# Optimization experiments

Hardware: AMD Instinct MI355X
Metric: run time of the kernel (lower is better)

Reference implementation:

```python
import jax, jax.numpy as jnp
import numpy as np

T, WQ, WS, C, H, W = 2, 75, 25, 640, 10, 10
WAY, SHOT = 5, 5
HID = C // 16
SCALE_VALUE = 30.0
ATTEN_SCALE_VALUE = 50.0
FROM_VALUE = 0.5
VALUE_INTERVAL = 0.3
BN_EPS = 1e-5
NORM_EPS = 1e-12


def _leaky(x):
    return jnp.where(x >= 0, x, 0.2 * x)


def _l2norm(x, axis):
    n = jnp.sqrt(jnp.sum(x * x, axis=axis, keepdims=True))
    return x / jnp.maximum(n, NORM_EPS)


def _embed(x, W_conv, bn_gamma, bn_beta, bn_mean, bn_var):
    # 1x1 conv (no bias) + eval-mode BatchNorm + LeakyReLU(0.2)
    # x: [t, n, c, h, w] -> [t, n, c, h, w]
    y = jnp.einsum('oc,tnchw->tnohw', W_conv, x)
    inv = bn_gamma / jnp.sqrt(bn_var + BN_EPS)
    y = y * inv[:, None, None] + (bn_beta - bn_mean * inv)[:, None, None]
    return _leaky(y)


def setup_inputs() -> dict:
    key = jax.random.key(0)
    ks = jax.random.split(key, 5)
    return {
        'query_feat': jax.random.normal(ks[0], (T, WQ, C, H, W), dtype=jnp.float32),
        'support_feat': jax.random.normal(ks[1], (T, WS, C, H, W), dtype=jnp.float32),
        'W_conv': jax.random.normal(ks[2], (C, C), dtype=jnp.float32) * 0.02,
        'bn_gamma': jnp.ones((C,), jnp.float32),
        'bn_beta': jnp.zeros((C,), jnp.float32),
        'bn_mean': jnp.zeros((C,), jnp.float32),
        'bn_var': jnp.ones((C,), jnp.float32),
        'psi_w1': jax.random.normal(ks[3], (C, HID), dtype=jnp.float32) * 0.04,
        'psi_b1': jnp.zeros((HID,), jnp.float32),
        'psi_w2': jax.random.normal(ks[4], (HID, 1), dtype=jnp.float32) * 0.15,
        'psi_b2': jnp.zeros((1,), jnp.float32),
        'way_num': WAY,
        'shot_num': SHOT,
    }


def reference(query_feat, support_feat, W_conv, bn_gamma, bn_beta, bn_mean, bn_var,
              psi_w1, psi_b1, psi_w2, psi_b2, way_num, shot_num):
    t, wq, c, h, w = query_feat.shape
    ws = support_feat.shape[1]
    hw = h * w

    # embedded + normalized features for the gated branch
    w_query = _embed(query_feat, W_conv, bn_gamma, bn_beta, bn_mean, bn_var)
    w_query = w_query.reshape(t, wq, c, hw).transpose(0, 1, 3, 2)      # [t, wq, hw, c]
    w_support = _embed(support_feat, W_conv, bn_gamma, bn_beta, bn_mean, bn_var)
    w_support = w_support.reshape(t, ws, c, hw).transpose(0, 2, 1, 3).reshape(t, c, ws * hw)
    w_query = _l2norm(w_query, axis=3)
    w_support = _l2norm(w_support, axis=1)

    # cosine similarity of embedded features: [t, wq, hw, ws*hw]
    f_x = jnp.einsum('tqpc,tck->tqpk', w_query, w_support)

    # AEAModule: per-location adaptive threshold from f_psi MLP
    hid = _leaky(w_query @ psi_w1 + psi_b1)                            # [t, wq, hw, HID]
    clamp_value = jax.nn.sigmoid(hid @ psi_w2 + psi_b2) * VALUE_INTERVAL + FROM_VALUE
    clamp_fx = jax.nn.sigmoid(ATTEN_SCALE_VALUE * (f_x - clamp_value))
    atten_score = clamp_fx / jnp.maximum(
        jnp.sum(jnp.abs(clamp_fx), axis=-1, keepdims=True), NORM_EPS)  # L1 normalize

    # raw-feature cosine similarity
    qf = _l2norm(query_feat.reshape(t, wq, c, hw).transpose(0, 1, 3, 2), axis=3)
    sf = _l2norm(support_feat.reshape(t, ws, c, hw).transpose(0, 2, 1, 3).reshape(t, c, ws * hw), axis=1)
    match_score = jnp.einsum('tqpc,tck->tqpk', qf, sf)                 # [t, wq, hw, ws*hw]

    # gate, regroup support axis into (way, shot, hw_s), reduce
    ams = (atten_score * match_score).reshape(t, wq, hw, way_num, shot_num, hw)
    score = ams.sum(axis=-1).mean(axis=(2, 4)) * SCALE_VALUE           # [t, wq, way]
    return score
```

## Files before the change

kernel.cpp:

```cpp
#include <hip/hip_runtime.h>
#include <stdint.h>

#define T_    2
#define WQ_   75
#define WS_   25
#define C_    640
#define HW_   100
#define HID_  40
#define WAY_  5
#define QP_   (WQ_*HW_)
#define SP_   (WS_*HW_)
#define NPT_  59
#define QT_   (NPT_*128)
#define KPAD_ 512
#define KROWS_ (WAY_*KPAD_)
#define C8_   (C_/8)
#define BM_   256

typedef _Float16 f16;
typedef _Float16 f16x8 __attribute__((ext_vector_type(8)));
typedef _Float16 f16x4 __attribute__((ext_vector_type(4)));
typedef _Float16 f16x16 __attribute__((ext_vector_type(16)));
typedef float    f32x4 __attribute__((ext_vector_type(4)));
typedef float    f32x16 __attribute__((ext_vector_type(16)));
typedef uint32_t u32;

__device__ __forceinline__ void gl_lds16(const f16* g, f16* l) {
  __builtin_amdgcn_global_load_lds(
      (const __attribute__((address_space(1))) u32*)g,
      (__attribute__((address_space(3))) u32*)l, 16, 0, 0);
}

__global__ __launch_bounds__(512) void k0_invnorm(
    const float* __restrict__ q, const float* __restrict__ s,
    float* __restrict__ rq_inv, float* __restrict__ rq_nrm,
    float* __restrict__ rs_inv, float* __restrict__ rs_nrm) {
  __shared__ float part[4][128];
  int b = blockIdx.x;
  int t = b / (WQ_ + WS_);
  int n = b % (WQ_ + WS_);
  int tid = threadIdx.x;
  int seg = tid >> 7, p = tid & 127;
  const float* base; float* oi; float* on; size_t idx;
  if (n < WQ_) {
    base = q + ((size_t)(t*WQ_ + n))*C_*HW_;
    idx = (size_t)t*QT_ + n*HW_ + p; oi = rq_inv; on = rq_nrm;
  } else {
    int m = n - WQ_;
    base = s + ((size_t)(t*WS_ + m))*C_*HW_;
    idx = (size_t)t*SP_ + m*HW_ + p; oi = rs_inv; on = rs_nrm;
  }
  float ss = 0.f;
  if (p < HW_) {
    for (int c = seg*160; c < seg*160 + 160; ++c) {
      float v = base[c*HW_ + p]; ss += v*v;
    }
  }
  part[seg][p] = ss;
  __syncthreads();
  if (seg == 0 && p < HW_) {
    float tot = part[0][p] + part[1][p] + part[2][p] + part[3][p];
    float nrm = fmaxf(sqrtf(tot), 1e-12f);
    oi[idx] = 1.f/nrm; on[idx] = nrm;
  }
}

__global__ __launch_bounds__(256) void kw_packW(
    const float* __restrict__ W, const float* __restrict__ w1,
    f16* __restrict__ Wr, f16* __restrict__ Wt8, f16* __restrict__ w1t) {
  int idx = blockIdx.x*256 + threadIdx.x;
  if (idx < C_*C8_) {
    int o = idx / C8_, c8 = idx % C8_;
    f16x8 v;
#pragma unroll
    for (int i = 0; i < 8; ++i) v[i] = (f16)W[(size_t)o*C_ + c8*8 + i];
    *reinterpret_cast<f16x8*>(Wr + (size_t)o*C_ + c8*8) = v;
    *reinterpret_cast<f16x8*>(Wt8 + ((size_t)c8*C_ + o)*8) = v;
  } else if (idx < C_*C8_ + 48*C8_) {
    int k2 = idx - C_*C8_;
    int h = k2 / C8_, c8 = k2 % C8_;
    f16x8 v;
#pragma unroll
    for (int i = 0; i < 8; ++i)
      v[i] = (h < HID_) ? (f16)w1[(size_t)(c8*8+i)*HID_ + h] : (f16)0.f;
    *reinterpret_cast<f16x8*>(w1t + (size_t)h*C_ + c8*8) = v;
  }
}

__global__ __launch_bounds__(256) void k1_pack_qraw(
    const float* __restrict__ q, const float* __restrict__ rq_inv,
    f16* __restrict__ Bq_raw) {
  int b = blockIdx.x;
  int ct = b % 10; b /= 10;
  int qq = b % WQ_; int t = b / WQ_;
  int c0 = ct*64;
  __shared__ float lds[64*HW_];
  const float4* s4 = reinterpret_cast<const float4*>(
      q + (((size_t)(t*WQ_ + qq))*C_ + c0)*HW_);
  float4* l4 = reinterpret_cast<float4*>(lds);
  for (int i = threadIdx.x; i < 64*HW_/4; i += 256) l4[i] = s4[i];
  __syncthreads();
  for (int ch = threadIdx.x; ch < 8*HW_; ch += 256) {
    int lc8 = ch / HW_, p = ch % HW_;
    float inv = rq_inv[(size_t)t*QT_ + qq*HW_ + p];
    f16x8 v;
#pragma unroll
    for (int i = 0; i < 8; ++i) v[i] = (f16)(lds[(lc8*8 + i)*HW_ + p] * inv);
    *reinterpret_cast<f16x8*>(
        Bq_raw + ((size_t)(t*C8_ + c0/8 + lc8)*QT_ + qq*HW_ + p)*8) = v;
  }
}

__global__ __launch_bounds__(256) void k2_pack_sraw(
    const float* __restrict__ s, const float* __restrict__ rs_inv,
    f16* __restrict__ As_raw) {
  int b = blockIdx.x;
  int ct = b % 10; b /= 10;
  int n = b % WS_; int t = b / WS_;
  int c0 = ct*64;
  __shared__ float lds[64*HW_];
  const float4* s4 = reinterpret_cast<const float4*>(
      s + (((size_t)(t*WS_ + n))*C_ + c0)*HW_);
  float4* l4 = reinterpret_cast<float4*>(lds);
  for (int i = threadIdx.x; i < 64*HW_/4; i += 256) l4[i] = s4[i];
  __syncthreads();
  for (int ch = threadIdx.x; ch < HW_*8; ch += 256) {
    int p = ch / 8, cc = ch % 8;
    float inv = rs_inv[t*SP_ + n*HW_ + p];
    f16x8 v;
#pragma unroll
    for (int i = 0; i < 8; ++i) v[i] = (f16)(lds[(cc*8 + i)*HW_ + p] * inv);
    int k = n*HW_ + p;
    int way = k / 500, ki = k % 500;
    size_t row = (size_t)way*KPAD_ + ki;
    *reinterpret_cast<f16x8*>(As_raw + ((size_t)(t*C8_ + c0/8 + cc)*KROWS_ + row)*8) = v;
  }
}

__global__ __launch_bounds__(512) void k3_embed_support(
    const f16* __restrict__ As_raw, const f16* __restrict__ Wt8,
    const float* __restrict__ rs_nrm,
    const float* __restrict__ g, const float* __restrict__ be,
    const float* __restrict__ mu, const float* __restrict__ va,
    f16* __restrict__ As_emb) {
  int b = blockIdx.x;
  int t = b / (KROWS_/32);
  int row0 = (b % (KROWS_/32)) * 32;
  int tid = threadIdx.x, wv = tid >> 6, lane = tid & 63;
  int mf = wv & 1, nh = wv >> 1;
  __shared__ f16 Alds[32*32];
  __shared__ f16 Blds[32*C_];
  __shared__ float rowss[32];
  f32x4 acc[10];
#pragma unroll
  for (int i = 0; i < 10; ++i) acc[i] = (f32x4){0.f,0.f,0.f,0.f};

  for (int cs = 0; cs < 20; ++cs) {
    if (tid < 128) {
      int c8l = tid >> 5, r = tid & 31;
      *reinterpret_cast<f16x8*>(Alds + (c8l*32 + r)*8) =
        *reinterpret_cast<const f16x8*>(
            As_raw + ((size_t)(t*C8_ + cs*4 + c8l)*KROWS_ + row0 + r)*8);
    }
    const f16x8* bsrc = reinterpret_cast<const f16x8*>(Wt8 + (size_t)(cs*4)*C_*8);
    f16x8* bdst = reinterpret_cast<f16x8*>(Blds);
    for (int i = tid; i < 4*C_; i += 512) bdst[i] = bsrc[i];
    __syncthreads();
    f16x8 a = *reinterpret_cast<const f16x8*>(
        Alds + ((lane>>4)*32 + mf*16 + (lane&15))*8);
#pragma unroll
    for (int nf = 0; nf < 10; ++nf) {
      int o = nh*160 + nf*16 + (lane & 15);
      f16x8 bf = *reinterpret_cast<const f16x8*>(Blds + (((lane>>4)*C_) + o)*8);
      acc[nf] = __builtin_amdgcn_mfma_f32_16x16x32_f16(a, bf, acc[nf], 0, 0, 0);
    }
    __syncthreads();
  }

  if (tid < 32) rowss[tid] = 0.f;
  __syncthreads();
  int rg = lane >> 4, cl = lane & 15;
  int lrow = mf*16 + rg*4;
  int prow = row0 + lrow;
#pragma unroll
  for (int j = 0; j < 4; ++j) {
    int pr = prow + j;
    int way = pr / KPAD_, ki = pr - way*KPAD_;
    bool valid = ki < 500;
    float nrm = valid ? rs_nrm[t*SP_ + way*500 + ki] : 0.f;
    float ssum = 0.f;
#pragma unroll
    for (int nf = 0; nf < 10; ++nf) {
      int o = nh*160 + nf*16 + cl;
      float inv = g[o] / sqrtf(va[o] + 1e-5f);
      float sh = be[o] - mu[o]*inv;
      float y = acc[nf][j]*nrm*inv + sh;
      y = (y >= 0.f) ? y : 0.2f*y;
      if (!valid) y = 0.f;
      acc[nf][j] = y;
      ssum += y*y;
    }
#pragma unroll
    for (int m = 1; m < 16; m <<= 1) ssum += __shfl_xor(ssum, m);
    if (cl == 0) atomicAdd(&rowss[lrow + j], ssum);
  }
  __syncthreads();
#pragma unroll
  for (int j = 0; j < 4; ++j) {
    int pr = prow + j;
    int ki = pr - (pr / KPAD_)*KPAD_;
    if (ki >= 500) continue;
    float invn = 1.f / fmaxf(sqrtf(rowss[lrow + j]), 1e-12f);
#pragma unroll
    for (int nf = 0; nf < 10; ++nf) {
      int o = nh*160 + nf*16 + cl;
      As_emb[((size_t)(t*C8_ + (o>>3))*KROWS_ + pr)*8 + (o&7)] = (f16)(acc[nf][j]*invn);
    }
  }
}

__global__ __launch_bounds__(256, 3) void k4_embed_query(
    const f16* __restrict__ Wr, const f16* __restrict__ Bq_raw,
    const float* __restrict__ rq_nrm,
    const float* __restrict__ g, const float* __restrict__ be,
    const float* __restrict__ mu, const float* __restrict__ va,
    f16* __restrict__ Bq_emb) {
  __shared__ f16 Ab[3][128*32];
  __shared__ f16 Bb[3][4*128*8];
  int b = blockIdx.x;
  int ot = b % 5; int m = b / 5;
  int pt = m % NPT_; int t = m / NPT_;
  int o0 = ot*128;
  int tid = threadIdx.x, w = tid >> 6, lane = tid & 63;
  int la_r = lane >> 2, la_c = lane & 3;

  auto stage = [&](int buf, int cs) {
#pragma unroll
    for (int i = 0; i < 2; ++i) {
      int ca = w*2 + i;
      int r = ca*16 + la_r;
      int sc = la_c ^ (r & 3);
      gl_lds16(Wr + (size_t)(o0 + r)*C_ + cs*32 + sc*8, &Ab[buf][ca*512]);
    }
#pragma unroll
    for (int i = 0; i < 2; ++i) {
      int cb = w*2 + i;
      int c8l = cb >> 1;
      size_t src = ((size_t)(t*C8_ + cs*4 + c8l)*QT_ + pt*128 + (cb&1)*64 + lane)*8;
      gl_lds16(Bq_raw + src, &Bb[buf][(c8l*128 + (cb&1)*64)*8]);
    }
  };

  f32x4 acc[2][8];
#pragma unroll
  for (int a = 0; a < 2; ++a)
#pragma unroll
    for (int n = 0; n < 8; ++n) acc[a][n] = (f32x4){0.f,0.f,0.f,0.f};

  stage(0, 0);
  stage(1, 1);
  for (int cs = 0; cs < 20; ++cs) {
    int buf = cs % 3;
    if (cs < 19) asm volatile("s_waitcnt vmcnt(4)" ::: "memory");
    else         asm volatile("s_waitcnt vmcnt(0)" ::: "memory");
    __builtin_amdgcn_s_barrier();
    if (cs < 18) stage((cs+2)%3, cs+2);
    __builtin_amdgcn_s_setprio(1);
    f16x8 fa[2];
#pragma unroll
    for (int mi = 0; mi < 2; ++mi) {
      int R = w*32 + mi*16 + (lane & 15);
      int sc = (lane >> 4) ^ (R & 3);
      fa[mi] = *reinterpret_cast<const f16x8*>(&Ab[buf][R*32 + sc*8]);
    }
#pragma unroll
    for (int nf = 0; nf < 8; ++nf) {
      f16x8 fb = *reinterpret_cast<const f16x8*>(
          &Bb[buf][((lane>>4)*128 + nf*16 + (lane&15))*8]);
#pragma unroll
      for (int mi = 0; mi < 2; ++mi)
        acc[mi][nf] = __builtin_amdgcn_mfma_f32_16x16x32_f16(fa[mi], fb, acc[mi][nf], 0, 0, 0);
    }
    __builtin_amdgcn_s_setprio(0);
  }

#pragma unroll
  for (int mi = 0; mi < 2; ++mi) {
    int obase = o0 + w*32 + mi*16 + (lane>>4)*4;
    float inv4[4], sh4[4];
#pragma unroll
    for (int j = 0; j < 4; ++j) {
      int o = obase + j;
      inv4[j] = g[o] / sqrtf(va[o] + 1e-5f);
      sh4[j] = be[o] - mu[o]*inv4[j];
    }
#pragma unroll
    for (int nf = 0; nf < 8; ++nf) {
      size_t gp = (size_t)pt*128 + nf*16 + (lane & 15);
      float nrmv = rq_nrm[(size_t)t*QT_ + gp];
      f16x4 vv;
#pragma unroll
      for (int j = 0; j < 4; ++j) {
        float y = (nrmv > 0.f) ? (acc[mi][nf][j]*nrmv*inv4[j] + sh4[j]) : 0.f;
        y = (y >= 0.f) ? y : 0.2f*y;
        vv[j] = (f16)y;
      }
      *reinterpret_cast<f16x4*>(
          &Bq_emb[((size_t)(t*C8_ + (obase>>3))*QT_ + gp)*8 + (obase&7)]) = vv;
    }
  }
}

__global__ __launch_bounds__(256) void k5_colnorm_psi(
    const f16* __restrict__ Bq_emb, const f16* __restrict__ w1t,
    const float* __restrict__ b1, const float* __restrict__ w2,
    const float* __restrict__ b2, float* __restrict__ cv,
    float* __restrict__ invq) {
  __shared__ float ssA[2][128];
  __shared__ float invs[128];
  __shared__ float hidL[48*128];
  int bq = blockIdx.x;
  int pt = bq % NPT_, t = bq / NPT_;
  int tid = threadIdx.x, w = tid >> 6, lane = tid & 63;
  size_t pbase = (size_t)pt*128;

  auto bptr = [&](int c8, int pp) -> const f16* {
    return Bq_emb + ((size_t)(t*C8_ + c8)*QT_ + pbase + pp)*8;
  };

  {
    int h2 = tid >> 7, pp = tid & 127;
    float ss = 0.f;
    for (int c8 = h2*40; c8 < h2*40 + 40; ++c8) {
      f16x8 v = *reinterpret_cast<const f16x8*>(bptr(c8, pp));
#pragma unroll
      for (int i = 0; i < 8; ++i) { float x = (float)v[i]; ss += x*x; }
    }
    ssA[h2][pp] = ss;
  }
  for (int i = tid; i < 48*128; i += 256) hidL[i] = 0.f;
  __syncthreads();
  if (tid < 128) {
    float ss = ssA[0][tid] + ssA[1][tid];
    float inv = (ss > 0.f) ? (1.f / fmaxf(sqrtf(ss), 1e-12f)) : 0.f;
    invs[tid] = inv;
    invq[(size_t)t*QT_ + pbase + tid] = inv;
  }

  f32x4 acc[3][8];
#pragma unroll
  for (int a = 0; a < 3; ++a)
#pragma unroll
    for (int n = 0; n < 8; ++n) acc[a][n] = (f32x4){0.f,0.f,0.f,0.f};
  for (int r = 0; r < 5; ++r) {
    int cs = w + r*4;
    f16x8 fa[3];
#pragma unroll
    for (int mf = 0; mf < 3; ++mf) {
      int R = mf*16 + (lane & 15);
      fa[mf] = *reinterpret_cast<const f16x8*>(&w1t[(size_t)R*C_ + cs*32 + (lane>>4)*8]);
    }
#pragma unroll
    for (int nf = 0; nf < 8; ++nf) {
      f16x8 fb = *reinterpret_cast<const f16x8*>(
          bptr(cs*4 + (lane>>4), nf*16 + (lane&15)));
#pragma unroll
      for (int mf = 0; mf < 3; ++mf)
        acc[mf][nf] = __builtin_amdgcn_mfma_f32_16x16x32_f16(fa[mf], fb, acc[mf][nf], 0, 0, 0);
    }
  }
  __syncthreads();
  for (int rr = 0; rr < 4; ++rr) {
    if (w == rr) {
#pragma unroll
      for (int mf = 0; mf < 3; ++mf)
#pragma unroll
        for (int nf = 0; nf < 8; ++nf)
#pragma unroll
          for (int j = 0; j < 4; ++j) {
            int row = mf*16 + (lane>>4)*4 + j;
            int col = nf*16 + (lane & 15);
            hidL[row*128 + col] += acc[mf][nf][j];
          }
    }
    __syncthreads();
  }
  if (tid < 128) {
    float inv = invs[tid];
    float z = b2[0];
    for (int h = 0; h < HID_; ++h) {
      float hv = hidL[h*128 + tid]*inv + b1[h];
      hv = (hv >= 0.f) ? hv : 0.2f*hv;
      z += hv*w2[h];
    }
    cv[(size_t)t*QT_ + pbase + tid] = 0.3f/(1.f + __expf(-z)) + 0.5f;
  }
}

__global__ __launch_bounds__(256, 2) void k6_main(
    const f16* __restrict__ As_emb, const f16* __restrict__ As_raw,
    const f16* __restrict__ Bq_emb, const f16* __restrict__ Bq_raw,
    const float* __restrict__ cv, const float* __restrict__ invq,
    float* __restrict__ Spart, float* __restrict__ L1part) {
  __shared__ f16 Ab[3][4*BM_*8];
  __shared__ f16 Bb[3][4*128*8];
  __shared__ float cvs[128], iqs[128], Ss[128], L1s[128];

  int bid = blockIdx.x;
  int xcd = bid & 7, j0 = bid >> 3;
  int l = (xcd < 4) ? xcd*148 + j0 : 592 + (xcd-4)*147 + j0;
  int wk = l % 10; int m = l / 10;
  int pt = m % NPT_; int t = m / NPT_;
  int way = wk >> 1, kt = wk & 1;

  int tid = threadIdx.x, w = tid >> 6, lane = tid & 63;
  if (tid < 128) {
    cvs[tid] = cv[(size_t)t*QT_ + pt*128 + tid];
    iqs[tid] = invq[(size_t)t*QT_ + pt*128 + tid];
    Ss[tid] = 0.f; L1s[tid] = 0.f;
  }
  int wrow0 = w*64;
  size_t rowb = (size_t)way*KPAD_ + (size_t)kt*BM_;

  const size_t aoff = ((size_t)(t*C8_ + w)*KROWS_ + rowb + lane)*8;
  const size_t boff = ((size_t)(t*C8_ + w)*QT_ + pt*128 + lane)*8;
  const f16* pA = As_raw + aoff;
  const f16* pB = Bq_raw + boff;
  const f16* pA1 = As_emb + aoff;
  const f16* pB1 = Bq_emb + boff;
  const int CS_A = 4*KROWS_*8;
  const int CS_B = 4*QT_*8;

  auto stage = [&](int buf, const f16* a, const f16* bsrc) {
    f16* da = &Ab[buf][(size_t)w*BM_*8];
    f16* db = &Bb[buf][(size_t)w*128*8];
    gl_lds16(a,        da);
    gl_lds16(a + 512,  da + 512);
    gl_lds16(a + 1024, da + 1024);
    gl_lds16(a + 1536, da + 1536);
    gl_lds16(bsrc,       db);
    gl_lds16(bsrc + 512, db + 512);
  };

  f32x16 acc[2][4];
  f16x16 mtc[2][4];
#pragma unroll
  for (int mi = 0; mi < 2; ++mi)
#pragma unroll
    for (int nf = 0; nf < 4; ++nf) acc[mi][nf] = (f32x16)(0.f);
  float Sl[4] = {0,0,0,0}, L1l[4] = {0,0,0,0};

  stage(0, pA, pB); pA += CS_A; pB += CS_B;
  stage(1, pA, pB); pA += CS_A; pB += CS_B;

  for (int ph = 0; ph < 40; ++ph) {
    if (ph == 18) { pA = pA1; pB = pB1; }
    int buf = ph % 3;
    if (ph < 39) asm volatile("s_waitcnt vmcnt(6)" ::: "memory");
    else         asm volatile("s_waitcnt vmcnt(0)" ::: "memory");
    __builtin_amdgcn_s_barrier();
    if (ph < 38) { stage((ph+2)%3, pA, pB); pA += CS_A; pB += CS_B; }
    __builtin_amdgcn_s_setprio(1);
    const f16* Abuf = Ab[buf];
    const f16* Bbuf = Bb[buf];
    int r0 = wrow0 + (lane & 31);
#pragma unroll
    for (int ks = 0; ks < 2; ++ks) {
      int c8l = ks*2 + (lane >> 5);
      f16x8 fa0 = *reinterpret_cast<const f16x8*>(&Abuf[(c8l*BM_ + r0)*8]);
      f16x8 fa1 = *reinterpret_cast<const f16x8*>(&Abuf[(c8l*BM_ + r0 + 32)*8]);
#pragma unroll
      for (int nf = 0; nf < 4; ++nf) {
        f16x8 fb = *reinterpret_cast<const f16x8*>(
            &Bbuf[(c8l*128 + nf*32 + (lane & 31))*8]);
        acc[0][nf] = __builtin_amdgcn_mfma_f32_32x32x16_f16(fa0, fb, acc[0][nf], 0, 0, 0);
        acc[1][nf] = __builtin_amdgcn_mfma_f32_32x32x16_f16(fa1, fb, acc[1][nf], 0, 0, 0);
      }
    }
    __builtin_amdgcn_s_setprio(0);

    if (ph == 19) {
#pragma unroll
      for (int mi = 0; mi < 2; ++mi)
#pragma unroll
        for (int nf = 0; nf < 4; ++nf)
#pragma unroll
          for (int jj = 0; jj < 16; ++jj) {
            mtc[mi][nf][jj] = (f16)fminf(fmaxf(acc[mi][nf][jj], -8.f), 8.f);
            acc[mi][nf][jj] = 0.f;
          }
    } else if (ph == 39) {
#pragma unroll
      for (int nf = 0; nf < 4; ++nf) {
        int col = nf*32 + (lane & 31);
        float cvv = cvs[col];
        float iq = iqs[col];
#pragma unroll
        for (int mi = 0; mi < 2; ++mi)
#pragma unroll
          for (int jj = 0; jj < 16; ++jj) {
            float fx = acc[mi][nf][jj] * iq;
            float sg = 1.f/(1.f + __expf(-50.f*(fx - cvv)));
            Sl[nf]  += sg * (float)mtc[mi][nf][jj];
            L1l[nf] += sg;
          }
      }
    }
  }

#pragma unroll
  for (int nf = 0; nf < 4; ++nf) {
    float vs = Sl[nf] + __shfl_xor(Sl[nf], 32);
    float vl = L1l[nf] + __shfl_xor(L1l[nf], 32);
    if (lane < 32) {
      atomicAdd(&Ss[nf*32 + lane], vs);
      atomicAdd(&L1s[nf*32 + lane], vl);
    }
  }
  __syncthreads();
  if (tid < 128) {
    size_t o = ((size_t)((t*WAY_ + way)*2 + kt))*QT_ + (size_t)pt*128 + tid;
    Spart[o] = Ss[tid]; L1part[o] = L1s[tid];
  }
}

__global__ __launch_bounds__(128) void k7_reduce(
    const float* __restrict__ Spart, const float* __restrict__ L1part,
    float* __restrict__ out) {
  int b = blockIdx.x;
  int t = b / WQ_, q = b % WQ_;
  int tid = threadIdx.x;
  __shared__ float red[128];
  float contrib[WAY_] = {0,0,0,0,0};
  if (tid < HW_) {
    size_t p = (size_t)t*0 + (size_t)q*HW_ + tid;
    float l1 = 0.f;
#pragma unroll
    for (int w = 0; w < WAY_; ++w)
#pragma unroll
      for (int k = 0; k < 2; ++k)
        l1 += L1part[((size_t)((t*WAY_ + w)*2 + k))*QT_ + p];
    l1 = fmaxf(l1, 1e-12f);
#pragma unroll
    for (int w = 0; w < WAY_; ++w) {
      float sv = 0.f;
#pragma unroll
      for (int k = 0; k < 2; ++k)
        sv += Spart[((size_t)((t*WAY_ + w)*2 + k))*QT_ + p];
      contrib[w] = sv / l1;
    }
  }
#pragma unroll
  for (int w = 0; w < WAY_; ++w) {
    red[tid] = contrib[w];
    __syncthreads();
    for (int off = 64; off > 0; off >>= 1) {
      if (tid < off) red[tid] += red[tid + off];
      __syncthreads();
    }
    if (tid == 0) out[b*WAY_ + w] = red[0] * 30.f / (float)(HW_*5);
    __syncthreads();
  }
}

extern "C" void kernel_launch(void* const* d_in, const int* in_sizes, int n_in,
                              void* d_out, int out_size, void* d_ws, size_t ws_size,
                              hipStream_t stream) {
  (void)in_sizes; (void)n_in; (void)out_size; (void)ws_size;
  const float* q  = (const float*)d_in[0];
  const float* s  = (const float*)d_in[1];
  const float* W  = (const float*)d_in[2];
  const float* g  = (const float*)d_in[3];
  const float* be = (const float*)d_in[4];
  const float* mu = (const float*)d_in[5];
  const float* va = (const float*)d_in[6];
  const float* w1 = (const float*)d_in[7];
  const float* b1 = (const float*)d_in[8];
  const float* w2 = (const float*)d_in[9];
  const float* b2 = (const float*)d_in[10];
  float* out = (float*)d_out;
  char* ws = (char*)d_ws;

  size_t off = 0;
  auto nxt = [&](size_t bytes) { size_t o = off; off += (bytes + 255) & ~(size_t)255; return o; };
  float* rq_inv = (float*)(ws + nxt((size_t)T_*QT_*4));
  float* rq_nrm = (float*)(ws + nxt((size_t)T_*QT_*4));
  float* rs_inv = (float*)(ws + nxt((size_t)T_*SP_*4));
  float* rs_nrm = (float*)(ws + nxt((size_t)T_*SP_*4));
  f16* Wr     = (f16*)(ws + nxt((size_t)C_*C_*2));
  f16* Wt8    = (f16*)(ws + nxt((size_t)C_*C_*2));
  f16* w1t    = (f16*)(ws + nxt((size_t)48*C_*2));
  f16* As_raw = (f16*)(ws + nxt((size_t)T_*KROWS_*C_*2));
  f16* As_emb = (f16*)(ws + nxt((size_t)T_*KROWS_*C_*2));
  f16* Bq_raw = (f16*)(ws + nxt((size_t)T_*C8_*QT_*8*2));
  f16* Bq_emb = (f16*)(ws + nxt((size_t)T_*C8_*QT_*8*2));
  float* cvp    = (float*)(ws + nxt((size_t)T_*QT_*4));
  float* invq   = (float*)(ws + nxt((size_t)T_*QT_*4));
  float* Spart  = (float*)(ws + nxt((size_t)T_*WAY_*2*QT_*4));
  float* L1part = (float*)(ws + nxt((size_t)T_*WAY_*2*QT_*4));

  hipMemsetAsync(As_raw, 0, (size_t)T_*KROWS_*C_*2, stream);
  hipMemsetAsync(As_emb, 0, (size_t)T_*KROWS_*C_*2, stream);
  hipMemsetAsync(Bq_raw, 0, (size_t)T_*C8_*QT_*8*2, stream);
  hipMemsetAsync(rq_inv, 0, (size_t)T_*QT_*4, stream);
  hipMemsetAsync(rq_nrm, 0, (size_t)T_*QT_*4, stream);

  k0_invnorm<<<T_*(WQ_+WS_), 512, 0, stream>>>(q, s, rq_inv, rq_nrm, rs_inv, rs_nrm);
  kw_packW<<<(C_*C8_ + 48*C8_ + 255)/256, 256, 0, stream>>>(W, w1, Wr, Wt8, w1t);
  k1_pack_qraw<<<T_*WQ_*10, 256, 0, stream>>>(q, rq_inv, Bq_raw);
  k2_pack_sraw<<<T_*WS_*10, 256, 0, stream>>>(s, rs_inv, As_raw);
  k3_embed_support<<<T_*(KROWS_/32), 512, 0, stream>>>(As_raw, Wt8, rs_nrm, g, be, mu, va, As_emb);
  k4_embed_query<<<T_*5*NPT_, 256, 0, stream>>>(Wr, Bq_raw, rq_nrm, g, be, mu, va, Bq_emb);
  k5_colnorm_psi<<<T_*NPT_, 256, 0, stream>>>(Bq_emb, w1t, b1, w2, b2, cvp, invq);
  k6_main<<<1180, 256, 0, stream>>>(As_emb, As_raw, Bq_emb, Bq_raw, cvp, invq, Spart, L1part);
  k7_reduce<<<T_*WQ_, 128, 0, stream>>>(Spart, L1part, out);
}
```

Measured before the change: 304.0 us.

## Widen main GEMM tile to 256x256 with 512-thread blocks and replace memsets

The main similarity kernel now computes a 256x256 output tile per block using 8 waves, which halves the number of blocks and doubles reuse of each staged A/B tile from LDS. The query padding is raised from 59 to 60 tiles of 128 so 256-wide tiles divide evenly, and the XCD block remapping is simplified. The full-buffer hipMemsetAsync calls are replaced by a small kernel that zeroes only the padding regions, and the support embed kernel now writes its padded rows instead of skipping them. Risks are lower occupancy (one block per CU) and some extra padded work.

```diff
diff --git a/kernel.cpp b/kernel.cpp
--- a/kernel.cpp
+++ b/kernel.cpp
@@ -10,12 +10,13 @@
 #define WAY_  5
 #define QP_   (WQ_*HW_)
 #define SP_   (WS_*HW_)
-#define NPT_  59
+#define NPT_  60
 #define QT_   (NPT_*128)
 #define KPAD_ 512
 #define KROWS_ (WAY_*KPAD_)
 #define C8_   (C_/8)
 #define BM_   256
+#define BN_   256
 
 typedef _Float16 f16;
 typedef _Float16 f16x8 __attribute__((ext_vector_type(8)));
@@ -29,6 +30,34 @@
   __builtin_amdgcn_global_load_lds(
       (const __attribute__((address_space(1))) u32*)g,
       (__attribute__((address_space(3))) u32*)l, 16, 0, 0);
+}
+
+__global__ __launch_bounds__(256) void kpad(
+    f16* __restrict__ Bq_raw, f16* __restrict__ As_raw,
+    float* __restrict__ rq_inv, float* __restrict__ rq_nrm) {
+  int idx = blockIdx.x*256 + threadIdx.x;
+  const float4 z4 = make_float4(0.f, 0.f, 0.f, 0.f);
+  if (idx < T_*C8_*(QT_-QP_)) {
+    int pp = idx % (QT_-QP_); int m = idx / (QT_-QP_);
+    int c8 = m % C8_; int t = m / C8_;
+    *reinterpret_cast<float4*>(Bq_raw + ((size_t)(t*C8_+c8)*QT_ + QP_ + pp)*8) = z4;
+    return;
+  }
+  int i2 = idx - T_*C8_*(QT_-QP_);
+  if (i2 < T_*C8_*WAY_*12) {
+    int r = i2 % 12; int m = i2 / 12;
+    int wy = m % WAY_; m /= WAY_;
+    int c8 = m % C8_; int t = m / C8_;
+    *reinterpret_cast<float4*>(
+        As_raw + ((size_t)(t*C8_+c8)*KROWS_ + (size_t)wy*KPAD_ + 500 + r)*8) = z4;
+    return;
+  }
+  int i3 = i2 - T_*C8_*WAY_*12;
+  if (i3 < T_*(QT_-QP_)) {
+    int pp = i3 % (QT_-QP_); int t = i3 / (QT_-QP_);
+    rq_inv[(size_t)t*QT_ + QP_ + pp] = 0.f;
+    rq_nrm[(size_t)t*QT_ + QP_ + pp] = 0.f;
+  }
 }
 
 __global__ __launch_bounds__(512) void k0_invnorm(
@@ -208,8 +237,6 @@
 #pragma unroll
   for (int j = 0; j < 4; ++j) {
     int pr = prow + j;
-    int ki = pr - (pr / KPAD_)*KPAD_;
-    if (ki >= 500) continue;
     float invn = 1.f / fmaxf(sqrtf(rowss[lrow + j]), 1e-12f);
 #pragma unroll
     for (int nf = 0; nf < 10; ++nf) {
@@ -397,33 +424,33 @@
   }
 }
 
-__global__ __launch_bounds__(256, 2) void k6_main(
+__global__ __launch_bounds__(512, 1) void k6_main(
     const f16* __restrict__ As_emb, const f16* __restrict__ As_raw,
     const f16* __restrict__ Bq_emb, const f16* __restrict__ Bq_raw,
     const float* __restrict__ cv, const float* __restrict__ invq,
     float* __restrict__ Spart, float* __restrict__ L1part) {
   __shared__ f16 Ab[3][4*BM_*8];
-  __shared__ f16 Bb[3][4*128*8];
-  __shared__ float cvs[128], iqs[128], Ss[128], L1s[128];
+  __shared__ f16 Bb[3][4*BN_*8];
+  __shared__ float cvs[BN_], iqs[BN_], Ss[BN_], L1s[BN_];
 
   int bid = blockIdx.x;
-  int xcd = bid & 7, j0 = bid >> 3;
-  int l = (xcd < 4) ? xcd*148 + j0 : 592 + (xcd-4)*147 + j0;
+  int l = (bid & 7)*75 + (bid >> 3);
   int wk = l % 10; int m = l / 10;
-  int pt = m % NPT_; int t = m / NPT_;
+  int pt = m % 30; int t = m / 30;
   int way = wk >> 1, kt = wk & 1;
 
   int tid = threadIdx.x, w = tid >> 6, lane = tid & 63;
-  if (tid < 128) {
-    cvs[tid] = cv[(size_t)t*QT_ + pt*128 + tid];
-    iqs[tid] = invq[(size_t)t*QT_ + pt*128 + tid];
+  if (tid < BN_) {
+    cvs[tid] = cv[(size_t)t*QT_ + pt*256 + tid];
+    iqs[tid] = invq[(size_t)t*QT_ + pt*256 + tid];
     Ss[tid] = 0.f; L1s[tid] = 0.f;
   }
-  int wrow0 = w*64;
+  int wr0 = (w & 3)*64;
+  int wc0 = (w >> 2)*128;
   size_t rowb = (size_t)way*KPAD_ + (size_t)kt*BM_;
 
-  const size_t aoff = ((size_t)(t*C8_ + w)*KROWS_ + rowb + lane)*8;
-  const size_t boff = ((size_t)(t*C8_ + w)*QT_ + pt*128 + lane)*8;
+  const size_t aoff = ((size_t)(t*C8_ + (w>>1))*KROWS_ + rowb + ((2*w)&3)*64 + lane)*8;
+  const size_t boff = ((size_t)(t*C8_ + (w>>1))*QT_ + (size_t)pt*256 + ((2*w)&3)*64 + lane)*8;
   const f16* pA = As_raw + aoff;
   const f16* pB = Bq_raw + boff;
   const f16* pA1 = As_emb + aoff;
@@ -432,14 +459,10 @@
   const int CS_B = 4*QT_*8;
 
   auto stage = [&](int buf, const f16* a, const f16* bsrc) {
-    f16* da = &Ab[buf][(size_t)w*BM_*8];
-    f16* db = &Bb[buf][(size_t)w*128*8];
-    gl_lds16(a,        da);
-    gl_lds16(a + 512,  da + 512);
-    gl_lds16(a + 1024, da + 1024);
-    gl_lds16(a + 1536, da + 1536);
-    gl_lds16(bsrc,       db);
-    gl_lds16(bsrc + 512, db + 512);
+    gl_lds16(a,       &Ab[buf][(2*w)*512]);
+    gl_lds16(a + 512, &Ab[buf][(2*w)*512 + 512]);
+    gl_lds16(bsrc,       &Bb[buf][(2*w)*512]);
+    gl_lds16(bsrc + 512, &Bb[buf][(2*w)*512 + 512]);
   };
 
   f32x16 acc[2][4];
@@ -456,14 +479,14 @@
   for (int ph = 0; ph < 40; ++ph) {
     if (ph == 18) { pA = pA1; pB = pB1; }
     int buf = ph % 3;
-    if (ph < 39) asm volatile("s_waitcnt vmcnt(6)" ::: "memory");
+    if (ph < 39) asm volatile("s_waitcnt vmcnt(4)" ::: "memory");
     else         asm volatile("s_waitcnt vmcnt(0)" ::: "memory");
     __builtin_amdgcn_s_barrier();
     if (ph < 38) { stage((ph+2)%3, pA, pB); pA += CS_A; pB += CS_B; }
     __builtin_amdgcn_s_setprio(1);
     const f16* Abuf = Ab[buf];
     const f16* Bbuf = Bb[buf];
-    int r0 = wrow0 + (lane & 31);
+    int r0 = wr0 + (lane & 31);
 #pragma unroll
     for (int ks = 0; ks < 2; ++ks) {
       int c8l = ks*2 + (lane >> 5);
@@ -472,7 +495,7 @@
 #pragma unroll
       for (int nf = 0; nf < 4; ++nf) {
         f16x8 fb = *reinterpret_cast<const f16x8*>(
-            &Bbuf[(c8l*128 + nf*32 + (lane & 31))*8]);
+            &Bbuf[(c8l*BN_ + wc0 + nf*32 + (lane & 31))*8]);
         acc[0][nf] = __builtin_amdgcn_mfma_f32_32x32x16_f16(fa0, fb, acc[0][nf], 0, 0, 0);
         acc[1][nf] = __builtin_amdgcn_mfma_f32_32x32x16_f16(fa1, fb, acc[1][nf], 0, 0, 0);
       }
@@ -492,7 +515,7 @@
     } else if (ph == 39) {
 #pragma unroll
       for (int nf = 0; nf < 4; ++nf) {
-        int col = nf*32 + (lane & 31);
+        int col = wc0 + nf*32 + (lane & 31);
         float cvv = cvs[col];
         float iq = iqs[col];
 #pragma unroll
@@ -513,13 +536,13 @@
     float vs = Sl[nf] + __shfl_xor(Sl[nf], 32);
     float vl = L1l[nf] + __shfl_xor(L1l[nf], 32);
     if (lane < 32) {
-      atomicAdd(&Ss[nf*32 + lane], vs);
-      atomicAdd(&L1s[nf*32 + lane], vl);
-    }
-  }
-  __syncthreads();
-  if (tid < 128) {
-    size_t o = ((size_t)((t*WAY_ + way)*2 + kt))*QT_ + (size_t)pt*128 + tid;
+      atomicAdd(&Ss[wc0 + nf*32 + lane], vs);
+      atomicAdd(&L1s[wc0 + nf*32 + lane], vl);
+    }
+  }
+  __syncthreads();
+  if (tid < BN_) {
+    size_t o = ((size_t)((t*WAY_ + way)*2 + kt))*QT_ + (size_t)pt*256 + tid;
     Spart[o] = Ss[tid]; L1part[o] = L1s[tid];
   }
 }
@@ -533,7 +556,7 @@
   __shared__ float red[128];
   float contrib[WAY_] = {0,0,0,0,0};
   if (tid < HW_) {
-    size_t p = (size_t)t*0 + (size_t)q*HW_ + tid;
+    size_t p = (size_t)q*HW_ + tid;
     float l1 = 0.f;
 #pragma unroll
     for (int w = 0; w < WAY_; ++w)
@@ -599,12 +622,8 @@
   float* Spart  = (float*)(ws + nxt((size_t)T_*WAY_*2*QT_*4));
   float* L1part = (float*)(ws + nxt((size_t)T_*WAY_*2*QT_*4));
 
-  hipMemsetAsync(As_raw, 0, (size_t)T_*KROWS_*C_*2, stream);
-  hipMemsetAsync(As_emb, 0, (size_t)T_*KROWS_*C_*2, stream);
-  hipMemsetAsync(Bq_raw, 0, (size_t)T_*C8_*QT_*8*2, stream);
-  hipMemsetAsync(rq_inv, 0, (size_t)T_*QT_*4, stream);
-  hipMemsetAsync(rq_nrm, 0, (size_t)T_*QT_*4, stream);
-
+  int padN = T_*C8_*(QT_-QP_) + T_*C8_*WAY_*12 + T_*(QT_-QP_);
+  kpad<<<(padN + 255)/256, 256, 0, stream>>>(Bq_raw, As_raw, rq_inv, rq_nrm);
   k0_invnorm<<<T_*(WQ_+WS_), 512, 0, stream>>>(q, s, rq_inv, rq_nrm, rs_inv, rs_nrm);
   kw_packW<<<(C_*C8_ + 48*C8_ + 255)/256, 256, 0, stream>>>(W, w1, Wr, Wt8, w1t);
   k1_pack_qraw<<<T_*WQ_*10, 256, 0, stream>>>(q, rq_inv, Bq_raw);
@@ -612,6 +631,6 @@
   k3_embed_support<<<T_*(KROWS_/32), 512, 0, stream>>>(As_raw, Wt8, rs_nrm, g, be, mu, va, As_emb);
   k4_embed_query<<<T_*5*NPT_, 256, 0, stream>>>(Wr, Bq_raw, rq_nrm, g, be, mu, va, Bq_emb);
   k5_colnorm_psi<<<T_*NPT_, 256, 0, stream>>>(Bq_emb, w1t, b1, w2, b2, cvp, invq);
-  k6_main<<<1180, 256, 0, stream>>>(As_emb, As_raw, Bq_emb, Bq_raw, cvp, invq, Spart, L1part);
+  k6_main<<<600, 512, 0, stream>>>(As_emb, As_raw, Bq_emb, Bq_raw, cvp, invq, Spart, L1part);
   k7_reduce<<<T_*WQ_, 128, 0, stream>>>(Spart, L1part, out);
 }
```

Result: slower. 315.0 us (+3.6%).

## Fuse setup kernels, replace full memsets with targeted pad zeroing

Applied to the files above, without the earlier changes.

Merges the norm computation, weight packing and padding-zeroing into a single setup kernel. The full-buffer memsets are replaced by writes to only the pad regions, and k3 now writes the padded support rows itself. NPT is raised to 60 so the 1200 main-kernel blocks split evenly across the 8 XCDs with a simpler mapping. This cuts launch count and memset traffic, but adds some padded query tiles of extra work.

```diff
diff --git a/kernel.cpp b/kernel.cpp
--- a/kernel.cpp
+++ b/kernel.cpp
@@ -10,12 +10,13 @@
 #define WAY_  5
 #define QP_   (WQ_*HW_)
 #define SP_   (WS_*HW_)
-#define NPT_  59
+#define NPT_  60
 #define QT_   (NPT_*128)
 #define KPAD_ 512
 #define KROWS_ (WAY_*KPAD_)
 #define C8_   (C_/8)
 #define BM_   256
+#define BNK_  128
 
 typedef _Float16 f16;
 typedef _Float16 f16x8 __attribute__((ext_vector_type(8)));
@@ -31,59 +32,95 @@
       (__attribute__((address_space(3))) u32*)l, 16, 0, 0);
 }
 
-__global__ __launch_bounds__(512) void k0_invnorm(
+#define NB0_ (T_*(WQ_+WS_))
+#define KWN_ (C_*C8_ + 48*C8_)
+#define NBW_ ((KWN_ + 511)/512)
+#define PADN_ (T_*C8_*(QT_-QP_) + T_*C8_*WAY_*12 + T_*(QT_-QP_))
+#define NBP_ ((PADN_ + 511)/512)
+
+__global__ __launch_bounds__(512) void ksetup(
     const float* __restrict__ q, const float* __restrict__ s,
+    const float* __restrict__ W, const float* __restrict__ w1,
     float* __restrict__ rq_inv, float* __restrict__ rq_nrm,
-    float* __restrict__ rs_inv, float* __restrict__ rs_nrm) {
-  __shared__ float part[4][128];
-  int b = blockIdx.x;
-  int t = b / (WQ_ + WS_);
-  int n = b % (WQ_ + WS_);
+    float* __restrict__ rs_inv, float* __restrict__ rs_nrm,
+    f16* __restrict__ Wr, f16* __restrict__ Wt8, f16* __restrict__ w1t,
+    f16* __restrict__ Bq_raw, f16* __restrict__ As_raw) {
+  int blk = blockIdx.x;
   int tid = threadIdx.x;
-  int seg = tid >> 7, p = tid & 127;
-  const float* base; float* oi; float* on; size_t idx;
-  if (n < WQ_) {
-    base = q + ((size_t)(t*WQ_ + n))*C_*HW_;
-    idx = (size_t)t*QT_ + n*HW_ + p; oi = rq_inv; on = rq_nrm;
-  } else {
-    int m = n - WQ_;
-    base = s + ((size_t)(t*WS_ + m))*C_*HW_;
-    idx = (size_t)t*SP_ + m*HW_ + p; oi = rs_inv; on = rs_nrm;
-  }
-  float ss = 0.f;
-  if (p < HW_) {
-    for (int c = seg*160; c < seg*160 + 160; ++c) {
-      float v = base[c*HW_ + p]; ss += v*v;
-    }
-  }
-  part[seg][p] = ss;
-  __syncthreads();
-  if (seg == 0 && p < HW_) {
-    float tot = part[0][p] + part[1][p] + part[2][p] + part[3][p];
-    float nrm = fmaxf(sqrtf(tot), 1e-12f);
-    oi[idx] = 1.f/nrm; on[idx] = nrm;
-  }
-}
-
-__global__ __launch_bounds__(256) void kw_packW(
-    const float* __restrict__ W, const float* __restrict__ w1,
-    f16* __restrict__ Wr, f16* __restrict__ Wt8, f16* __restrict__ w1t) {
-  int idx = blockIdx.x*256 + threadIdx.x;
-  if (idx < C_*C8_) {
-    int o = idx / C8_, c8 = idx % C8_;
-    f16x8 v;
-#pragma unroll
-    for (int i = 0; i < 8; ++i) v[i] = (f16)W[(size_t)o*C_ + c8*8 + i];
-    *reinterpret_cast<f16x8*>(Wr + (size_t)o*C_ + c8*8) = v;
-    *reinterpret_cast<f16x8*>(Wt8 + ((size_t)c8*C_ + o)*8) = v;
-  } else if (idx < C_*C8_ + 48*C8_) {
-    int k2 = idx - C_*C8_;
-    int h = k2 / C8_, c8 = k2 % C8_;
-    f16x8 v;
-#pragma unroll
-    for (int i = 0; i < 8; ++i)
-      v[i] = (h < HID_) ? (f16)w1[(size_t)(c8*8+i)*HID_ + h] : (f16)0.f;
-    *reinterpret_cast<f16x8*>(w1t + (size_t)h*C_ + c8*8) = v;
+
+  if (blk < NB0_) {
+    __shared__ float part[4][128];
+    int t = blk / (WQ_ + WS_);
+    int n = blk % (WQ_ + WS_);
+    int seg = tid >> 7, p = tid & 127;
+    const float* base; float* oi; float* on; size_t idx;
+    if (n < WQ_) {
+      base = q + ((size_t)(t*WQ_ + n))*C_*HW_;
+      idx = (size_t)t*QT_ + n*HW_ + p; oi = rq_inv; on = rq_nrm;
+    } else {
+      int m = n - WQ_;
+      base = s + ((size_t)(t*WS_ + m))*C_*HW_;
+      idx = (size_t)t*SP_ + m*HW_ + p; oi = rs_inv; on = rs_nrm;
+    }
+    float ss = 0.f;
+    if (p < HW_) {
+      for (int c = seg*160; c < seg*160 + 160; ++c) {
+        float v = base[c*HW_ + p]; ss += v*v;
+      }
+    }
+    part[seg][p] = ss;
+    __syncthreads();
+    if (seg == 0 && p < HW_) {
+      float tot = part[0][p] + part[1][p] + part[2][p] + part[3][p];
+      float nrm = fmaxf(sqrtf(tot), 1e-12f);
+      oi[idx] = 1.f/nrm; on[idx] = nrm;
+    }
+    return;
+  }
+  if (blk < NB0_ + NBW_) {
+    int idx = (blk - NB0_)*512 + tid;
+    if (idx < C_*C8_) {
+      int o = idx / C8_, c8 = idx % C8_;
+      f16x8 v;
+#pragma unroll
+      for (int i = 0; i < 8; ++i) v[i] = (f16)W[(size_t)o*C_ + c8*8 + i];
+      *reinterpret_cast<f16x8*>(Wr + (size_t)o*C_ + c8*8) = v;
+      *reinterpret_cast<f16x8*>(Wt8 + ((size_t)c8*C_ + o)*8) = v;
+    } else if (idx < KWN_) {
+      int k2 = idx - C_*C8_;
+      int h = k2 / C8_, c8 = k2 % C8_;
+      f16x8 v;
+#pragma unroll
+      for (int i = 0; i < 8; ++i)
+        v[i] = (h < HID_) ? (f16)w1[(size_t)(c8*8+i)*HID_ + h] : (f16)0.f;
+      *reinterpret_cast<f16x8*>(w1t + (size_t)h*C_ + c8*8) = v;
+    }
+    return;
+  }
+  {
+    int idx = (blk - NB0_ - NBW_)*512 + tid;
+    const float4 z4 = make_float4(0.f, 0.f, 0.f, 0.f);
+    if (idx < T_*C8_*(QT_-QP_)) {
+      int pp = idx % (QT_-QP_); int m = idx / (QT_-QP_);
+      int c8 = m % C8_; int t = m / C8_;
+      *reinterpret_cast<float4*>(Bq_raw + ((size_t)(t*C8_+c8)*QT_ + QP_ + pp)*8) = z4;
+      return;
+    }
+    int i2 = idx - T_*C8_*(QT_-QP_);
+    if (i2 < T_*C8_*WAY_*12) {
+      int r = i2 % 12; int m = i2 / 12;
+      int wy = m % WAY_; m /= WAY_;
+      int c8 = m % C8_; int t = m / C8_;
+      *reinterpret_cast<float4*>(
+          As_raw + ((size_t)(t*C8_+c8)*KROWS_ + (size_t)wy*KPAD_ + 500 + r)*8) = z4;
+      return;
+    }
+    int i3 = i2 - T_*C8_*WAY_*12;
+    if (i3 < T_*(QT_-QP_)) {
+      int pp = i3 % (QT_-QP_); int t = i3 / (QT_-QP_);
+      rq_inv[(size_t)t*QT_ + QP_ + pp] = 0.f;
+      rq_nrm[(size_t)t*QT_ + QP_ + pp] = 0.f;
+    }
   }
 }
 
@@ -208,8 +245,6 @@
 #pragma unroll
   for (int j = 0; j < 4; ++j) {
     int pr = prow + j;
-    int ki = pr - (pr / KPAD_)*KPAD_;
-    if (ki >= 500) continue;
     float invn = 1.f / fmaxf(sqrtf(rowss[lrow + j]), 1e-12f);
 #pragma unroll
     for (int nf = 0; nf < 10; ++nf) {
@@ -403,18 +438,17 @@
     const float* __restrict__ cv, const float* __restrict__ invq,
     float* __restrict__ Spart, float* __restrict__ L1part) {
   __shared__ f16 Ab[3][4*BM_*8];
-  __shared__ f16 Bb[3][4*128*8];
-  __shared__ float cvs[128], iqs[128], Ss[128], L1s[128];
+  __shared__ f16 Bb[3][4*BNK_*8];
+  __shared__ float cvs[BNK_], iqs[BNK_], Ss[BNK_], L1s[BNK_];
 
   int bid = blockIdx.x;
-  int xcd = bid & 7, j0 = bid >> 3;
-  int l = (xcd < 4) ? xcd*148 + j0 : 592 + (xcd-4)*147 + j0;
+  int l = (bid & 7)*150 + (bid >> 3);
   int wk = l % 10; int m = l / 10;
   int pt = m % NPT_; int t = m / NPT_;
   int way = wk >> 1, kt = wk & 1;
 
   int tid = threadIdx.x, w = tid >> 6, lane = tid & 63;
-  if (tid < 128) {
+  if (tid < BNK_) {
     cvs[tid] = cv[(size_t)t*QT_ + pt*128 + tid];
     iqs[tid] = invq[(size_t)t*QT_ + pt*128 + tid];
     Ss[tid] = 0.f; L1s[tid] = 0.f;
@@ -423,7 +457,7 @@
   size_t rowb = (size_t)way*KPAD_ + (size_t)kt*BM_;
 
   const size_t aoff = ((size_t)(t*C8_ + w)*KROWS_ + rowb + lane)*8;
-  const size_t boff = ((size_t)(t*C8_ + w)*QT_ + pt*128 + lane)*8;
+  const size_t boff = ((size_t)(t*C8_ + w)*QT_ + (size_t)pt*128 + lane)*8;
   const f16* pA = As_raw + aoff;
   const f16* pB = Bq_raw + boff;
   const f16* pA1 = As_emb + aoff;
@@ -433,7 +467,7 @@
 
   auto stage = [&](int buf, const f16* a, const f16* bsrc) {
     f16* da = &Ab[buf][(size_t)w*BM_*8];
-    f16* db = &Bb[buf][(size_t)w*128*8];
+    f16* db = &Bb[buf][(size_t)w*BNK_*8];
     gl_lds16(a,        da);
     gl_lds16(a + 512,  da + 512);
     gl_lds16(a + 1024, da + 1024);
@@ -472,7 +506,7 @@
 #pragma unroll
       for (int nf = 0; nf < 4; ++nf) {
         f16x8 fb = *reinterpret_cast<const f16x8*>(
-            &Bbuf[(c8l*128 + nf*32 + (lane & 31))*8]);
+            &Bbuf[(c8l*BNK_ + nf*32 + (lane & 31))*8]);
         acc[0][nf] = __builtin_amdgcn_mfma_f32_32x32x16_f16(fa0, fb, acc[0][nf], 0, 0, 0);
         acc[1][nf] = __builtin_amdgcn_mfma_f32_32x32x16_f16(fa1, fb, acc[1][nf], 0, 0, 0);
       }
@@ -518,7 +552,7 @@
     }
   }
   __syncthreads();
-  if (tid < 128) {
+  if (tid < BNK_) {
     size_t o = ((size_t)((t*WAY_ + way)*2 + kt))*QT_ + (size_t)pt*128 + tid;
     Spart[o] = Ss[tid]; L1part[o] = L1s[tid];
   }
@@ -533,7 +567,7 @@
   __shared__ float red[128];
   float contrib[WAY_] = {0,0,0,0,0};
   if (tid < HW_) {
-    size_t p = (size_t)t*0 + (size_t)q*HW_ + tid;
+    size_t p = (size_t)q*HW_ + tid;
     float l1 = 0.f;
 #pragma unroll
     for (int w = 0; w < WAY_; ++w)
@@ -599,19 +633,13 @@
   float* Spart  = (float*)(ws + nxt((size_t)T_*WAY_*2*QT_*4));
   float* L1part = (float*)(ws + nxt((size_t)T_*WAY_*2*QT_*4));
 
-  hipMemsetAsync(As_raw, 0, (size_t)T_*KROWS_*C_*2, stream);
-  hipMemsetAsync(As_emb, 0, (size_t)T_*KROWS_*C_*2, stream);
-  hipMemsetAsync(Bq_raw, 0, (size_t)T_*C8_*QT_*8*2, stream);
-  hipMemsetAsync(rq_inv, 0, (size_t)T_*QT_*4, stream);
-  hipMemsetAsync(rq_nrm, 0, (size_t)T_*QT_*4, stream);
-
-  k0_invnorm<<<T_*(WQ_+WS_), 512, 0, stream>>>(q, s, rq_inv, rq_nrm, rs_inv, rs_nrm);
-  kw_packW<<<(C_*C8_ + 48*C8_ + 255)/256, 256, 0, stream>>>(W, w1, Wr, Wt8, w1t);
+  ksetup<<<NB0_ + NBW_ + NBP_, 512, 0, stream>>>(
+      q, s, W, w1, rq_inv, rq_nrm, rs_inv, rs_nrm, Wr, Wt8, w1t, Bq_raw, As_raw);
   k1_pack_qraw<<<T_*WQ_*10, 256, 0, stream>>>(q, rq_inv, Bq_raw);
   k2_pack_sraw<<<T_*WS_*10, 256, 0, stream>>>(s, rs_inv, As_raw);
   k3_embed_support<<<T_*(KROWS_/32), 512, 0, stream>>>(As_raw, Wt8, rs_nrm, g, be, mu, va, As_emb);
   k4_embed_query<<<T_*5*NPT_, 256, 0, stream>>>(Wr, Bq_raw, rq_nrm, g, be, mu, va, Bq_emb);
   k5_colnorm_psi<<<T_*NPT_, 256, 0, stream>>>(Bq_emb, w1t, b1, w2, b2, cvp, invq);
-  k6_main<<<1180, 256, 0, stream>>>(As_emb, As_raw, Bq_emb, Bq_raw, cvp, invq, Spart, L1part);
+  k6_main<<<1200, 256, 0, stream>>>(As_emb, As_raw, Bq_emb, Bq_raw, cvp, invq, Spart, L1part);
   k7_reduce<<<T_*WQ_, 128, 0, stream>>>(Spart, L1part, out);
 }
```

Result: faster. 283.7 us (median of 2 runs) (-6.7%).
